# Optimization experiments

Measured on AMD Instinct MI355X. Metric: run time of the kernel, lower is better.

Reference implementation:

```python
import jax, jax.numpy as jnp
import numpy as np

S, B, H, NH = 2048, 1, 4096, 32
HD = H // NH            # 128
ROT = int(HD * 0.25)    # 32 partial rotary dims
BASE = 10000.0


def setup_inputs() -> dict:
    key = jax.random.key(0)
    ks = jax.random.split(key, 4)
    hidden_states = jax.random.normal(ks[0], (S, B, H), dtype=jnp.float32)
    W_qkv = jax.random.normal(ks[1], (3 * H, H), dtype=jnp.float32) * 0.02
    b_qkv = jnp.zeros((3 * H,), dtype=jnp.float32)
    W_dense = jax.random.normal(ks[2], (H, H), dtype=jnp.float32) * 0.02
    b_dense = jnp.zeros((H,), dtype=jnp.float32)
    # causal left-to-right mask, True = attend
    attention_mask = jnp.tril(jnp.ones((S, S), dtype=bool))[None, None]  # [1,1,S,S]
    return dict(hidden_states=hidden_states, attention_mask=attention_mask,
                W_qkv=W_qkv, b_qkv=b_qkv, W_dense=W_dense, b_dense=b_dense)


def _rotate_half(x):
    x1, x2 = jnp.split(x, 2, axis=-1)
    return jnp.concatenate((-x2, x1), axis=-1)


def reference(hidden_states, attention_mask, W_qkv, b_qkv, W_dense, b_dense):
    S_, B_ = hidden_states.shape[:2]
    qkv = hidden_states @ W_qkv.T + b_qkv                    # [S,B,3H]
    qkv = qkv.reshape(S_, B_, NH, 3 * HD)
    q, k, v = qkv[..., :HD], qkv[..., HD:2 * HD], qkv[..., 2 * HD:]

    # partial rotary embedding (GPT-NeoX style, offset=0, no KV cache)
    inv_freq = 1.0 / (BASE ** (jnp.arange(0, ROT, 2, dtype=jnp.float32) / ROT))
    t = jnp.arange(S_, dtype=jnp.float32)
    freqs = jnp.einsum('s,d->sd', t, inv_freq)               # [S,ROT/2]
    emb = jnp.concatenate((freqs, freqs), axis=-1)           # [S,ROT]
    cos = jnp.cos(emb)[:, None, None, :]                     # [S,1,1,ROT]
    sin = jnp.sin(emb)[:, None, None, :]

    def rope(x):
        return x * cos + _rotate_half(x) * sin

    q = jnp.concatenate((rope(q[..., :ROT]), q[..., ROT:]), axis=-1)
    k = jnp.concatenate((rope(k[..., :ROT]), k[..., ROT:]), axis=-1)

    # scaled dot-product attention with explicit score matrix
    scores = jnp.einsum('sbhd,tbhd->bhst', q, k) / np.float32(np.sqrt(HD))
    scores = jnp.where(attention_mask, scores, jnp.float32(-10000.0))
    probs = jax.nn.softmax(scores, axis=-1)                  # [B,NH,S,S]
    ctx = jnp.einsum('bhst,tbhd->sbhd', probs, v).reshape(S_, B_, H)
    return ctx @ W_dense.T + b_dense                         # [S,B,H]
```

## Files before the change

### kernel.cpp

```cpp
#include <hip/hip_runtime.h>
#include <hip/hip_bf16.h>
#include <math.h>

typedef __bf16 bf16_t;
typedef bf16_t bf16x8 __attribute__((ext_vector_type(8)));
typedef bf16_t bf16x4 __attribute__((ext_vector_type(4)));
typedef float floatx4 __attribute__((ext_vector_type(4)));

#define S_LEN 2048
#define QK_LD 8192

__global__ void convert_all(const float* __restrict__ a, bf16_t* __restrict__ ao,
                            const float* __restrict__ b, bf16_t* __restrict__ bo,
                            const float* __restrict__ c, bf16_t* __restrict__ co) {
    int i = blockIdx.x * 256 + threadIdx.x;
    const float* src; bf16_t* dst; int j;
    if (i < 2097152)        { src = a; dst = ao; j = i; }
    else if (i < 14680064)  { src = b; dst = bo; j = i - 2097152; }
    else                    { src = c; dst = co; j = i - 14680064; }
    float4 v = ((const float4*)src)[j];
    bf16x4 o;
    o.x = (bf16_t)v.x; o.y = (bf16_t)v.y; o.z = (bf16_t)v.z; o.w = (bf16_t)v.w;
    ((bf16x4*)dst)[j] = o;
}

__device__ __forceinline__ void async_copy16(const void* g, void* l) {
    __builtin_amdgcn_global_load_lds(
        (const __attribute__((address_space(1))) unsigned int*)g,
        (__attribute__((address_space(3))) unsigned int*)l, 16, 0, 0);
}

__global__ __launch_bounds__(256) void qkv_gemm(
    const bf16_t* __restrict__ A, const bf16_t* __restrict__ B,
    const float* __restrict__ bias, bf16_t* __restrict__ qkout,
    bf16_t* __restrict__ vt)
{
    __shared__ bf16_t As[128 * 32];
    __shared__ bf16_t Bs[128 * 32];
    const int K = 4096;
    const int t    = threadIdx.x;
    const int lane = t & 63;
    const int w    = t >> 6;
    const int l15  = lane & 15;
    const int quad = lane >> 4;
    const int bm = blockIdx.y, bn = blockIdx.x;
    const int mw = (w >> 1) * 64, nw = (w & 1) * 64;

    floatx4 acc[4][4];
    #pragma unroll
    for (int i = 0; i < 4; i++)
        #pragma unroll
        for (int j = 0; j < 4; j++)
            acc[i][j] = (floatx4){0.f, 0.f, 0.f, 0.f};

    const int r0 = t >> 2;
    const int c0 = (t & 3) * 8;
    const bf16_t* Aptr = A + (size_t)(bm * 128 + r0) * K + c0;
    const bf16_t* Bptr = B + (size_t)(bn * 128 + r0) * K + c0;
    bf16_t* AsW = As + t * 8;
    bf16_t* BsW = Bs + t * 8;

    for (int k0 = 0; k0 < K; k0 += 32) {
        __syncthreads();
        async_copy16(Aptr + k0, AsW);
        async_copy16(Aptr + k0 + (size_t)64 * K, AsW + 2048);
        async_copy16(Bptr + k0, BsW);
        async_copy16(Bptr + k0 + (size_t)64 * K, BsW + 2048);
        __syncthreads();

        bf16x8 a[4], b[4];
        #pragma unroll
        for (int mi = 0; mi < 4; mi++)
            a[mi] = *(const bf16x8*)&As[(mw + mi * 16 + l15) * 32 + quad * 8];
        #pragma unroll
        for (int ni = 0; ni < 4; ni++)
            b[ni] = *(const bf16x8*)&Bs[(nw + ni * 16 + l15) * 32 + quad * 8];
        #pragma unroll
        for (int mi = 0; mi < 4; mi++)
            #pragma unroll
            for (int ni = 0; ni < 4; ni++)
                acc[mi][ni] = __builtin_amdgcn_mfma_f32_16x16x32_bf16(a[mi], b[ni], acc[mi][ni], 0, 0, 0);
    }

    #pragma unroll
    for (int ni = 0; ni < 4; ni++) {
        float bv = bias[bn * 128 + nw + ni * 16 + l15];
        #pragma unroll
        for (int mi = 0; mi < 4; mi++)
            #pragma unroll
            for (int r = 0; r < 4; r++)
                acc[mi][ni][r] += bv;
    }

    const int h = bn / 3, ht = bn - h * 3;
    if (ht < 2) {
        if (nw == 0) {
            float invf = exp2f(-(float)l15 * 0.8304820237218405f);
            #pragma unroll
            for (int mi = 0; mi < 4; mi++)
                #pragma unroll
                for (int r = 0; r < 4; r++) {
                    int s = bm * 128 + mw + mi * 16 + quad * 4 + r;
                    float sn, cs;
                    sincosf((float)s * invf, &sn, &cs);
                    float x1 = acc[mi][0][r], x2 = acc[mi][1][r];
                    acc[mi][0][r] = x1 * cs - x2 * sn;
                    acc[mi][1][r] = x2 * cs + x1 * sn;
                }
        }
        bf16_t* base = qkout + h * 256 + ht * 128;
        #pragma unroll
        for (int mi = 0; mi < 4; mi++)
            #pragma unroll
            for (int ni = 0; ni < 4; ni++) {
                int col = nw + ni * 16 + l15;
                #pragma unroll
                for (int r = 0; r < 4; r++) {
                    int row = bm * 128 + mw + mi * 16 + quad * 4 + r;
                    base[(size_t)row * QK_LD + col] = (bf16_t)acc[mi][ni][r];
                }
            }
    } else {
        bf16_t* vbase = vt + (size_t)h * 128 * S_LEN;
        #pragma unroll
        for (int mi = 0; mi < 4; mi++) {
            int s0 = bm * 128 + mw + mi * 16 + quad * 4;
            #pragma unroll
            for (int ni = 0; ni < 4; ni++) {
                int d = nw + ni * 16 + l15;
                bf16x4 pv;
                #pragma unroll
                for (int r = 0; r < 4; r++) pv[r] = (bf16_t)acc[mi][ni][r];
                *(bf16x4*)&vbase[(size_t)d * S_LEN + s0] = pv;
            }
        }
    }
}

__global__ __launch_bounds__(256) void dense_gemm(
    const bf16_t* __restrict__ A, const bf16_t* __restrict__ B,
    const float* __restrict__ bias, float* __restrict__ C,
    int M, int N, int K)
{
    __shared__ bf16_t As[128 * 32];
    __shared__ bf16_t Bs[128 * 32];
    const int t    = threadIdx.x;
    const int lane = t & 63;
    const int w    = t >> 6;
    const int l15  = lane & 15;
    const int quad = lane >> 4;
    const int bm = blockIdx.y, bn = blockIdx.x;
    const int mw = (w >> 1) * 64, nw = (w & 1) * 64;

    floatx4 acc[4][4];
    #pragma unroll
    for (int i = 0; i < 4; i++)
        #pragma unroll
        for (int j = 0; j < 4; j++)
            acc[i][j] = (floatx4){0.f, 0.f, 0.f, 0.f};

    const int r0 = t >> 2;
    const int c0 = (t & 3) * 8;
    const bf16_t* Aptr = A + (size_t)(bm * 128 + r0) * K + c0;
    const bf16_t* Bptr = B + (size_t)(bn * 128 + r0) * K + c0;
    bf16_t* AsW = As + t * 8;
    bf16_t* BsW = Bs + t * 8;

    for (int k0 = 0; k0 < K; k0 += 32) {
        __syncthreads();
        async_copy16(Aptr + k0, AsW);
        async_copy16(Aptr + k0 + (size_t)64 * K, AsW + 2048);
        async_copy16(Bptr + k0, BsW);
        async_copy16(Bptr + k0 + (size_t)64 * K, BsW + 2048);
        __syncthreads();

        bf16x8 a[4], b[4];
        #pragma unroll
        for (int mi = 0; mi < 4; mi++)
            a[mi] = *(const bf16x8*)&As[(mw + mi * 16 + l15) * 32 + quad * 8];
        #pragma unroll
        for (int ni = 0; ni < 4; ni++)
            b[ni] = *(const bf16x8*)&Bs[(nw + ni * 16 + l15) * 32 + quad * 8];
        #pragma unroll
        for (int mi = 0; mi < 4; mi++)
            #pragma unroll
            for (int ni = 0; ni < 4; ni++)
                acc[mi][ni] = __builtin_amdgcn_mfma_f32_16x16x32_bf16(a[mi], b[ni], acc[mi][ni], 0, 0, 0);
    }

    #pragma unroll
    for (int ni = 0; ni < 4; ni++) {
        float bv = bias[bn * 128 + nw + ni * 16 + l15];
        int col = bn * 128 + nw + ni * 16 + l15;
        #pragma unroll
        for (int mi = 0; mi < 4; mi++)
            #pragma unroll
            for (int r = 0; r < 4; r++) {
                int row = bm * 128 + mw + mi * 16 + quad * 4 + r;
                C[(size_t)row * N + col] = acc[mi][ni][r] + bv;
            }
    }
}

#define QK_LDS 136
#define V_LDS  72
__global__ __launch_bounds__(256) void flash_attn(
    const bf16_t* __restrict__ qk, const bf16_t* __restrict__ Vt,
    bf16_t* __restrict__ ctx)
{
    __shared__ bf16_t Qs[64 * QK_LDS];
    __shared__ bf16_t Ks[64 * QK_LDS];
    __shared__ bf16_t Vs[128 * V_LDS];
    __shared__ bf16_t Ps[64 * V_LDS];
    const int h = blockIdx.y;
    const int qb = (int)gridDim.x - 1 - blockIdx.x;
    const int t = threadIdx.x;
    const int w = t >> 6, lane = t & 63;
    const int quad = lane >> 4, l15 = lane & 15;
    const float L2E = 1.4426950408889634f;
    const float ISQ = 0.08838834764831845f;

    {
        const bf16_t* qbase = qk + (size_t)(qb * 64) * QK_LD + h * 256;
        int rr = t >> 4, cc = (t & 15) * 8;
        #pragma unroll
        for (int p = 0; p < 4; p++) {
            int row = rr + p * 16;
            *(bf16x8*)&Qs[row * QK_LDS + cc] = *(const bf16x8*)&qbase[(size_t)row * QK_LD + cc];
        }
    }

    floatx4 o[8];
    #pragma unroll
    for (int i = 0; i < 8; i++) o[i] = (floatx4){0.f, 0.f, 0.f, 0.f};
    float mrow[4] = {-1e30f, -1e30f, -1e30f, -1e30f};
    float lrow[4] = {0.f, 0.f, 0.f, 0.f};

    for (int kt = 0; kt <= qb; kt++) {
        __syncthreads();
        {
            const bf16_t* kbase = qk + (size_t)(kt * 64) * QK_LD + h * 256 + 128;
            int rr = t >> 4, cc = (t & 15) * 8;
            #pragma unroll
            for (int p = 0; p < 4; p++) {
                int row = rr + p * 16;
                *(bf16x8*)&Ks[row * QK_LDS + cc] = *(const bf16x8*)&kbase[(size_t)row * QK_LD + cc];
            }
            const bf16_t* vbase = Vt + (size_t)h * 128 * S_LEN + kt * 64;
            int vr = t >> 3, vc = (t & 7) * 8;
            #pragma unroll
            for (int p = 0; p < 4; p++) {
                int row = vr + p * 32;
                *(bf16x8*)&Vs[row * V_LDS + vc] = *(const bf16x8*)&vbase[(size_t)row * S_LEN + vc];
            }
        }
        __syncthreads();

        floatx4 sacc[4];
        #pragma unroll
        for (int ni = 0; ni < 4; ni++) sacc[ni] = (floatx4){0.f, 0.f, 0.f, 0.f};
        #pragma unroll
        for (int ks = 0; ks < 4; ks++) {
            bf16x8 aq = *(const bf16x8*)&Qs[(w * 16 + l15) * QK_LDS + ks * 32 + quad * 8];
            #pragma unroll
            for (int ni = 0; ni < 4; ni++) {
                bf16x8 bk = *(const bf16x8*)&Ks[(ni * 16 + l15) * QK_LDS + ks * 32 + quad * 8];
                sacc[ni] = __builtin_amdgcn_mfma_f32_16x16x32_bf16(aq, bk, sacc[ni], 0, 0, 0);
            }
        }

        float p_[4][4];
        #pragma unroll
        for (int ni = 0; ni < 4; ni++)
            #pragma unroll
            for (int r = 0; r < 4; r++)
                p_[ni][r] = sacc[ni][r] * ISQ;
        if (kt == qb) {
            #pragma unroll
            for (int ni = 0; ni < 4; ni++) {
                int key = ni * 16 + l15;
                #pragma unroll
                for (int r = 0; r < 4; r++)
                    if (key > w * 16 + quad * 4 + r) p_[ni][r] = -1e30f;
            }
        }

        float alpha[4];
        #pragma unroll
        for (int r = 0; r < 4; r++) {
            float mx = fmaxf(fmaxf(p_[0][r], p_[1][r]), fmaxf(p_[2][r], p_[3][r]));
            #pragma unroll
            for (int off = 1; off < 16; off <<= 1)
                mx = fmaxf(mx, __shfl_xor(mx, off, 16));
            float mnew = fmaxf(mrow[r], mx);
            alpha[r] = __builtin_amdgcn_exp2f((mrow[r] - mnew) * L2E);
            mrow[r] = mnew;
        }
        float lad[4] = {0.f, 0.f, 0.f, 0.f};
        #pragma unroll
        for (int ni = 0; ni < 4; ni++)
            #pragma unroll
            for (int r = 0; r < 4; r++) {
                float pv = __builtin_amdgcn_exp2f((p_[ni][r] - mrow[r]) * L2E);
                p_[ni][r] = pv;
                lad[r] += pv;
            }
        #pragma unroll
        for (int r = 0; r < 4; r++) {
            #pragma unroll
            for (int off = 1; off < 16; off <<= 1)
                lad[r] += __shfl_xor(lad[r], off, 16);
            lrow[r] = lrow[r] * alpha[r] + lad[r];
        }
        #pragma unroll
        for (int ni = 0; ni < 8; ni++)
            #pragma unroll
            for (int r = 0; r < 4; r++)
                o[ni][r] *= alpha[r];

        #pragma unroll
        for (int ni = 0; ni < 4; ni++)
            #pragma unroll
            for (int r = 0; r < 4; r++)
                Ps[(w * 16 + quad * 4 + r) * V_LDS + ni * 16 + l15] = (bf16_t)p_[ni][r];
        asm volatile("s_waitcnt lgkmcnt(0)" ::: "memory");

        #pragma unroll
        for (int ks = 0; ks < 2; ks++) {
            bf16x8 ap = *(const bf16x8*)&Ps[(w * 16 + l15) * V_LDS + ks * 32 + quad * 8];
            #pragma unroll
            for (int ni = 0; ni < 8; ni++) {
                bf16x8 bv = *(const bf16x8*)&Vs[(ni * 16 + l15) * V_LDS + ks * 32 + quad * 8];
                o[ni] = __builtin_amdgcn_mfma_f32_16x16x32_bf16(ap, bv, o[ni], 0, 0, 0);
            }
        }
    }

    float invl[4];
    #pragma unroll
    for (int r = 0; r < 4; r++) invl[r] = 1.f / lrow[r];
    bf16_t* cbase = ctx + (size_t)(qb * 64) * 4096 + h * 128;
    #pragma unroll
    for (int ni = 0; ni < 8; ni++) {
        int col = ni * 16 + l15;
        #pragma unroll
        for (int r = 0; r < 4; r++) {
            int row = w * 16 + quad * 4 + r;
            cbase[(size_t)row * 4096 + col] = (bf16_t)(o[ni][r] * invl[r]);
        }
    }
}

extern "C" void kernel_launch(void* const* d_in, const int* in_sizes, int n_in,
                              void* d_out, int out_size, void* d_ws, size_t ws_size,
                              hipStream_t stream) {
    const float* hidden = (const float*)d_in[0];
    const float* Wqkv   = (const float*)d_in[2];
    const float* bqkv   = (const float*)d_in[3];
    const float* Wd     = (const float*)d_in[4];
    const float* bd     = (const float*)d_in[5];
    float* out = (float*)d_out;

    char* ws = (char*)d_ws;
    bf16_t* h_bf    = (bf16_t*)(ws);
    bf16_t* wqkv_bf = (bf16_t*)(ws + 16777216);
    bf16_t* wd_bf   = (bf16_t*)(ws + 117440512);
    bf16_t* qk      = (bf16_t*)(ws + 150994944);
    bf16_t* vt      = (bf16_t*)(ws + 184549376);
    bf16_t* ctx     = (bf16_t*)(ws + 201326592);

    convert_all<<<73728, 256, 0, stream>>>(hidden, h_bf, Wqkv, wqkv_bf, Wd, wd_bf);
    qkv_gemm<<<dim3(96, 16), 256, 0, stream>>>(h_bf, wqkv_bf, bqkv, qk, vt);
    flash_attn<<<dim3(32, 32), 256, 0, stream>>>(qk, vt, ctx);
    dense_gemm<<<dim3(32, 16), 256, 0, stream>>>(ctx, wd_bf, bd, out, 2048, 4096, 4096);
}
```

Baseline: 933.6 us.

## Split-K dense projection with atomic accumulation and bias-initialized output; fast sincos

The output projection GEMM is split along K into two halves across a new grid dimension, and each half accumulates into the output with atomic float adds. The conversion kernel is extended to pre-fill the output with the bias. This doubles the number of blocks to improve CU utilization, at the cost of atomic traffic and nondeterministic summation order. The rotary embedding's sincosf is replaced with range-reduced hardware sin/cos instructions to cut transcendental cost, with slightly lower precision.

```diff
diff --git a/kernel.cpp b/kernel.cpp
--- a/kernel.cpp
+++ b/kernel.cpp
@@ -12,8 +12,14 @@
 
 __global__ void convert_all(const float* __restrict__ a, bf16_t* __restrict__ ao,
                             const float* __restrict__ b, bf16_t* __restrict__ bo,
-                            const float* __restrict__ c, bf16_t* __restrict__ co) {
+                            const float* __restrict__ c, bf16_t* __restrict__ co,
+                            const float* __restrict__ bias, float* __restrict__ outv) {
     int i = blockIdx.x * 256 + threadIdx.x;
+    if (i >= 18874368) {
+        int j = i - 18874368;
+        ((float4*)outv)[j] = ((const float4*)bias)[j & 1023];
+        return;
+    }
     const float* src; bf16_t* dst; int j;
     if (i < 2097152)        { src = a; dst = ao; j = i; }
     else if (i < 14680064)  { src = b; dst = bo; j = i - 2097152; }
@@ -28,6 +34,13 @@
     __builtin_amdgcn_global_load_lds(
         (const __attribute__((address_space(1))) unsigned int*)g,
         (__attribute__((address_space(3))) unsigned int*)l, 16, 0, 0);
+}
+
+__device__ __forceinline__ void fast_sincos(float x, float* sn, float* cs) {
+    float rev = x * 0.15915494309189535f;
+    rev = rev - floorf(rev);
+    *sn = __builtin_amdgcn_sinf(rev);
+    *cs = __builtin_amdgcn_cosf(rev);
 }
 
 __global__ __launch_bounds__(256) void qkv_gemm(
@@ -102,7 +115,7 @@
                 for (int r = 0; r < 4; r++) {
                     int s = bm * 128 + mw + mi * 16 + quad * 4 + r;
                     float sn, cs;
-                    sincosf((float)s * invf, &sn, &cs);
+                    fast_sincos((float)s * invf, &sn, &cs);
                     float x1 = acc[mi][0][r], x2 = acc[mi][1][r];
                     acc[mi][0][r] = x1 * cs - x2 * sn;
                     acc[mi][1][r] = x2 * cs + x1 * sn;
@@ -137,10 +150,9 @@
     }
 }
 
-__global__ __launch_bounds__(256) void dense_gemm(
+__global__ __launch_bounds__(256) void dense_gemm_sk(
     const bf16_t* __restrict__ A, const bf16_t* __restrict__ B,
-    const float* __restrict__ bias, float* __restrict__ C,
-    int M, int N, int K)
+    float* __restrict__ C, int M, int N, int K)
 {
     __shared__ bf16_t As[128 * 32];
     __shared__ bf16_t Bs[128 * 32];
@@ -150,6 +162,7 @@
     const int l15  = lane & 15;
     const int quad = lane >> 4;
     const int bm = blockIdx.y, bn = blockIdx.x;
+    const int kc = blockIdx.z;
     const int mw = (w >> 1) * 64, nw = (w & 1) * 64;
 
     floatx4 acc[4][4];
@@ -160,13 +173,13 @@
             acc[i][j] = (floatx4){0.f, 0.f, 0.f, 0.f};
 
     const int r0 = t >> 2;
-    const int c0 = (t & 3) * 8;
+    const int c0 = (t & 3) * 8 + kc * 2048;
     const bf16_t* Aptr = A + (size_t)(bm * 128 + r0) * K + c0;
     const bf16_t* Bptr = B + (size_t)(bn * 128 + r0) * K + c0;
     bf16_t* AsW = As + t * 8;
     bf16_t* BsW = Bs + t * 8;
 
-    for (int k0 = 0; k0 < K; k0 += 32) {
+    for (int k0 = 0; k0 < 2048; k0 += 32) {
         __syncthreads();
         async_copy16(Aptr + k0, AsW);
         async_copy16(Aptr + k0 + (size_t)64 * K, AsW + 2048);
@@ -190,14 +203,13 @@
 
     #pragma unroll
     for (int ni = 0; ni < 4; ni++) {
-        float bv = bias[bn * 128 + nw + ni * 16 + l15];
         int col = bn * 128 + nw + ni * 16 + l15;
         #pragma unroll
         for (int mi = 0; mi < 4; mi++)
             #pragma unroll
             for (int r = 0; r < 4; r++) {
                 int row = bm * 128 + mw + mi * 16 + quad * 4 + r;
-                C[(size_t)row * N + col] = acc[mi][ni][r] + bv;
+                unsafeAtomicAdd(&C[(size_t)row * N + col], acc[mi][ni][r]);
             }
     }
 }
@@ -369,8 +381,8 @@
     bf16_t* vt      = (bf16_t*)(ws + 184549376);
     bf16_t* ctx     = (bf16_t*)(ws + 201326592);
 
-    convert_all<<<73728, 256, 0, stream>>>(hidden, h_bf, Wqkv, wqkv_bf, Wd, wd_bf);
+    convert_all<<<81920, 256, 0, stream>>>(hidden, h_bf, Wqkv, wqkv_bf, Wd, wd_bf, bd, out);
     qkv_gemm<<<dim3(96, 16), 256, 0, stream>>>(h_bf, wqkv_bf, bqkv, qk, vt);
     flash_attn<<<dim3(32, 32), 256, 0, stream>>>(qk, vt, ctx);
-    dense_gemm<<<dim3(32, 16), 256, 0, stream>>>(ctx, wd_bf, bd, out, 2048, 4096, 4096);
-}
+    dense_gemm_sk<<<dim3(32, 16, 2), 256, 0, stream>>>(ctx, wd_bf, out, 2048, 4096, 4096);
+}
```

Result: slower. 966.4 us (+3.5%).
